# Kernel tuning notes

Hardware: AMD Instinct MI355X
Metric: run time of the kernel (lower is better)

The kernel has to match this reference:

```python
import jax, jax.numpy as jnp
import numpy as np

NZ, N_GEN = 128, 10
H1, H2, IMG = 512, 1024, 784
BATCH = 4096


def setup_inputs() -> dict:
    key = jax.random.key(0)
    ks = jax.random.split(key, 5)
    z = jax.random.normal(ks[0], (BATCH, NZ), dtype=jnp.float32)
    g_idx = jax.random.randint(ks[1], (BATCH,), 0, N_GEN)
    # stacked per-generator MLP weights (fan-in scaled init)
    W1 = jax.random.normal(ks[2], (N_GEN, NZ, H1), dtype=jnp.float32) / np.sqrt(NZ)
    b1 = jnp.zeros((N_GEN, H1), dtype=jnp.float32)
    W2 = jax.random.normal(ks[3], (N_GEN, H1, H2), dtype=jnp.float32) / np.sqrt(H1)
    b2 = jnp.zeros((N_GEN, H2), dtype=jnp.float32)
    W3 = jax.random.normal(ks[4], (N_GEN, H2, IMG), dtype=jnp.float32) / np.sqrt(H2)
    b3 = jnp.zeros((N_GEN, IMG), dtype=jnp.float32)
    return {"z": z, "g_idx": g_idx, "W1": W1, "b1": b1, "W2": W2, "b2": b2, "W3": W3, "b3": b3}


def reference(z, g_idx, W1, b1, W2, b2, W3, b3):
    # Run ALL n_gen sub-generators for every sample (as the torch module does),
    # then gather the chosen branch per sample.
    h = jax.nn.relu(jnp.einsum('bz,gzh->bgh', z, W1) + b1)          # [B, G, H1]
    h = jax.nn.relu(jnp.einsum('bgh,ghk->bgk', h, W2) + b2)         # [B, G, H2]
    images = jnp.tanh(jnp.einsum('bgk,gki->bgi', h, W3) + b3)       # [B, G, IMG]
    # images[arange(B), g_idx]
    out = jnp.take_along_axis(images, g_idx[:, None, None], axis=1)[:, 0]  # [B, IMG]
    return out
```

## Files before the change

### kernel.cpp

```cpp
#include <hip/hip_runtime.h>
#include <math.h>

#define NZ    128
#define H1    512
#define H2    1024
#define IMG   784
#define IMGP  832
#define BATCH 4096
#define NGEN  10
#define MPAD  128

typedef _Float16 f16;
typedef __attribute__((ext_vector_type(8))) _Float16 half8;
typedef __attribute__((ext_vector_type(4))) float floatx4;

__device__ __forceinline__ void cp16(void* l, const void* g) {
    __builtin_amdgcn_global_load_lds((const __attribute__((address_space(1))) void*)g,
                                     (__attribute__((address_space(3))) void*)l, 16, 0, 0);
}

__global__ __launch_bounds__(1024)
void hist_perm(const int* __restrict__ g_idx, int* __restrict__ seg,
               int* __restrict__ perm) {
    __shared__ int lc[NGEN];
    __shared__ int lb[NGEN + 1];
    const int t = threadIdx.x;
    if (t < NGEN) lc[t] = 0;
    __syncthreads();
    int gv[BATCH / 1024];
    #pragma unroll
    for (int i = 0; i < BATCH / 1024; ++i) {
        gv[i] = g_idx[t + i * 1024];
        atomicAdd(&lc[gv[i]], 1);
    }
    __syncthreads();
    if (t == 0) {
        int s = 0;
        for (int g = 0; g < NGEN; ++g) { lb[g] = s; s += lc[g]; }
        lb[NGEN] = s;
    }
    __syncthreads();
    if (t <= NGEN) seg[t] = lb[t];
    if (t < NGEN) lc[t] = lb[t];
    __syncthreads();
    #pragma unroll
    for (int i = 0; i < BATCH / 1024; ++i) {
        int p = atomicAdd(&lc[gv[i]], 1);
        perm[p] = t + i * 1024;
    }
}

__global__ void pack_z(const float* __restrict__ z, const int* __restrict__ perm,
                       f16* __restrict__ zp) {
    const int i = blockIdx.x * 256 + threadIdx.x;
    const int r = i >> 5, c = (i & 31) * 4;
    const int s = perm[r];
    float4 v = *(const float4*)(z + (size_t)s * NZ + c);
    union { ushort4 u; f16 h[4]; } o;
    o.h[0] = (f16)v.x; o.h[1] = (f16)v.y; o.h[2] = (f16)v.z; o.h[3] = (f16)v.w;
    *(ushort4*)(zp + (size_t)r * NZ + c) = o.u;
}

template<int K, int N, int NPAD>
__global__ __launch_bounds__(256)
void transpose_f16(const float* __restrict__ W, f16* __restrict__ Wt) {
    const int g  = blockIdx.z;
    const int k0 = blockIdx.x * 32;
    const int n0 = blockIdx.y * 32;
    __shared__ f16 L[32][36];
    const int t = threadIdx.x;
    {
        const int kk = t >> 3;
        const int nq = (t & 7) * 4;
        float4 v = make_float4(0.f, 0.f, 0.f, 0.f);
        if (n0 + nq < N)
            v = *(const float4*)(W + ((size_t)g * K + (k0 + kk)) * N + n0 + nq);
        L[nq + 0][kk] = (f16)v.x;
        L[nq + 1][kk] = (f16)v.y;
        L[nq + 2][kk] = (f16)v.z;
        L[nq + 3][kk] = (f16)v.w;
    }
    __syncthreads();
    {
        const int nn = t >> 3;
        const int kq = (t & 7) * 4;
        *(ushort4*)(Wt + ((size_t)g * NPAD + (n0 + nn)) * K + k0 + kq) =
            *(const ushort4*)&L[nn][kq];
    }
}

template<int K, int NOUT, int NPADB, int ACT, int SCATTER>
__global__ __launch_bounds__(256)
void gemm64(const f16* __restrict__ Ap, const f16* __restrict__ Wt,
            const float* __restrict__ bias, f16* __restrict__ Ch,
            float* __restrict__ Cout, const int* __restrict__ seg,
            const int* __restrict__ perm) {
    const int g  = blockIdx.z;
    const int s0 = seg[g];
    const int ng = seg[g + 1] - s0;
    const int m0 = blockIdx.x * 64;
    if (m0 >= ng) return;
    const int n0 = blockIdx.y * 64;

    __shared__ f16 As[64 * 64];
    __shared__ f16 Bs[64 * 64];

    const int tid = threadIdx.x, lane = tid & 63, w = tid >> 6;

    const f16* ga[2]; const f16* gb[2]; f16* la[2]; f16* lb[2];
    #pragma unroll
    for (int j = 0; j < 2; ++j) {
        const int r   = w * 16 + j * 8 + (lane >> 3);
        const int swz = ((lane & 7) ^ ((r >> 1) & 7)) * 8;
        ga[j] = Ap + (size_t)(s0 + m0 + r) * K + swz;
        gb[j] = Wt + ((size_t)g * NPADB + n0 + r) * K + swz;
        la[j] = As + (w * 16 + j * 8) * 64;
        lb[j] = Bs + (w * 16 + j * 8) * 64;
    }

    const int wm = (w & 1) * 32, wn = (w >> 1) * 32;
    const int lm = lane & 15, lq = lane >> 4;

    floatx4 acc[2][2] = {};

    #pragma unroll
    for (int kc = 0; kc < K / 64; ++kc) {
        __syncthreads();
        #pragma unroll
        for (int j = 0; j < 2; ++j) {
            cp16(la[j], ga[j]); cp16(lb[j], gb[j]);
            ga[j] += 64; gb[j] += 64;
        }
        __syncthreads();
        #pragma unroll
        for (int ks = 0; ks < 2; ++ks) {
            half8 a[2], b[2];
            #pragma unroll
            for (int mt = 0; mt < 2; ++mt) {
                const int r  = wm + mt * 16 + lm;
                const int pq = (ks * 4 + lq) ^ ((r >> 1) & 7);
                a[mt] = *(const half8*)&As[r * 64 + pq * 8];
            }
            #pragma unroll
            for (int nf = 0; nf < 2; ++nf) {
                const int r  = wn + 2 * lm + nf;
                const int pq = (ks * 4 + lq) ^ ((r >> 1) & 7);
                b[nf] = *(const half8*)&Bs[r * 64 + pq * 8];
            }
            #pragma unroll
            for (int mt = 0; mt < 2; ++mt)
                #pragma unroll
                for (int nf = 0; nf < 2; ++nf)
                    acc[mt][nf] = __builtin_amdgcn_mfma_f32_16x16x32_f16(
                        a[mt], b[nf], acc[mt][nf], 0, 0, 0);
        }
    }

    const int c = n0 + wn + 2 * lm;
    const float b0 = (c     < NOUT) ? bias[(size_t)g * NOUT + c]     : 0.f;
    const float b1 = (c + 1 < NOUT) ? bias[(size_t)g * NOUT + c + 1] : 0.f;
    #pragma unroll
    for (int mt = 0; mt < 2; ++mt)
        #pragma unroll
        for (int rr = 0; rr < 4; ++rr) {
            const int gr = m0 + wm + mt * 16 + lq * 4 + rr;
            if (gr >= ng) continue;
            float x0 = acc[mt][0][rr] + b0;
            float x1 = acc[mt][1][rr] + b1;
            if (ACT == 0) {
                x0 = fmaxf(x0, 0.f); x1 = fmaxf(x1, 0.f);
            } else {
                const float e0 = __expf(2.f * x0);
                const float e1 = __expf(2.f * x1);
                x0 = 1.f - 2.f / (e0 + 1.f);
                x1 = 1.f - 2.f / (e1 + 1.f);
            }
            if (SCATTER) {
                if (c < NOUT) {
                    const size_t orow = (size_t)perm[s0 + gr];
                    *(float2*)&Cout[orow * NOUT + c] = make_float2(x0, x1);
                }
            } else {
                union { uint u; f16 h[2]; } o;
                o.h[0] = (f16)x0; o.h[1] = (f16)x1;
                *(uint*)&Ch[(size_t)(s0 + gr) * NOUT + c] = o.u;
            }
        }
}

extern "C" void kernel_launch(void* const* d_in, const int* in_sizes, int n_in,
                              void* d_out, int out_size, void* d_ws, size_t ws_size,
                              hipStream_t stream) {
    const float* z    = (const float*)d_in[0];
    const int*   gidx = (const int*)  d_in[1];
    const float* W1   = (const float*)d_in[2];
    const float* b1   = (const float*)d_in[3];
    const float* W2   = (const float*)d_in[4];
    const float* b2   = (const float*)d_in[5];
    const float* W3   = (const float*)d_in[6];
    const float* b3   = (const float*)d_in[7];
    float* out = (float*)d_out;

    char* ws = (char*)d_ws;
    size_t off = 0;
    auto alloc = [&](size_t bytes) { size_t o = off; off = (off + bytes + 255) & ~255ULL; return o; };
    int* seg  = (int*)(ws + alloc((size_t)(NGEN + 1) * 4));
    int* perm = (int*)(ws + alloc((size_t)(BATCH + MPAD) * 4));
    f16* zp  = (f16*)(ws + alloc((size_t)(BATCH + MPAD) * NZ * 2));
    f16* h1p = (f16*)(ws + alloc((size_t)(BATCH + MPAD) * H1 * 2));
    f16* h2p = (f16*)(ws + alloc((size_t)(BATCH + MPAD) * H2 * 2));
    f16* W1t = (f16*)(ws + alloc((size_t)NGEN * H1 * NZ * 2));
    f16* W2t = (f16*)(ws + alloc((size_t)NGEN * H2 * H1 * 2));
    f16* W3t = (f16*)(ws + alloc((size_t)NGEN * IMGP * H2 * 2));

    hist_perm<<<dim3(1), dim3(1024), 0, stream>>>(gidx, seg, perm);
    pack_z<<<dim3(BATCH * (NZ / 4) / 256), dim3(256), 0, stream>>>(z, perm, zp);
    transpose_f16<NZ, H1, H1><<<dim3(NZ / 32, H1 / 32, NGEN), dim3(256), 0, stream>>>(W1, W1t);
    transpose_f16<H1, H2, H2><<<dim3(H1 / 32, H2 / 32, NGEN), dim3(256), 0, stream>>>(W2, W2t);
    transpose_f16<H2, IMG, IMGP><<<dim3(H2 / 32, IMGP / 32, NGEN), dim3(256), 0, stream>>>(W3, W3t);

    gemm64<NZ, H1, H1, 0, 0><<<dim3(16, H1 / 64, NGEN), dim3(256), 0, stream>>>(
        zp, W1t, b1, h1p, nullptr, seg, perm);
    gemm64<H1, H2, H2, 0, 0><<<dim3(16, H2 / 64, NGEN), dim3(256), 0, stream>>>(
        h1p, W2t, b2, h2p, nullptr, seg, perm);
    gemm64<H2, IMG, IMGP, 1, 1><<<dim3(16, IMGP / 64, NGEN), dim3(256), 0, stream>>>(
        h2p, W3t, b3, nullptr, out, seg, perm);
}
```

Measured before the change: 181.2 us.

## Double-buffer GEMM LDS tiles and merge weight transposes into one launch

The GEMM main loop now uses two LDS buffers per operand. It prefetches the next K-chunk with global_load_lds while the current one feeds the MFMAs, and uses explicit waitcnt and barriers in place of the two __syncthreads per iteration. The three per-layer weight transpose kernels are fused into a single launch that dispatches tiles by block index. This targets global-load latency inside the GEMMs and the overhead of separate launches. In exchange it doubles LDS use per block and relies on hand-coded waitcnt immediates being correct.

After: 187.3 us. +3.4%, slower.

```diff
diff --git a/kernel.cpp b/kernel.cpp
--- a/kernel.cpp
+++ b/kernel.cpp
@@ -62,11 +62,10 @@
 }
 
 template<int K, int N, int NPAD>
-__global__ __launch_bounds__(256)
-void transpose_f16(const float* __restrict__ W, f16* __restrict__ Wt) {
-    const int g  = blockIdx.z;
-    const int k0 = blockIdx.x * 32;
-    const int n0 = blockIdx.y * 32;
+__device__ __forceinline__
+void trans_tile(const float* __restrict__ W, f16* __restrict__ Wt,
+                int kb, int nb, int g) {
+    const int k0 = kb * 32, n0 = nb * 32;
     __shared__ f16 L[32][36];
     const int t = threadIdx.x;
     {
@@ -89,12 +88,33 @@
     }
 }
 
+#define T1 ((NZ / 32) * (H1 / 32))
+#define T2 ((H1 / 32) * (H2 / 32))
+#define T3 ((H2 / 32) * (IMGP / 32))
+__global__ __launch_bounds__(256)
+void transpose_all(const float* __restrict__ W1, const float* __restrict__ W2,
+                   const float* __restrict__ W3, f16* __restrict__ W1t,
+                   f16* __restrict__ W2t, f16* __restrict__ W3t) {
+    const int g = blockIdx.z;
+    const int x = blockIdx.x;
+    if (x < T1) {
+        trans_tile<NZ, H1, H1>(W1, W1t, x % (NZ / 32), x / (NZ / 32), g);
+    } else if (x < T1 + T2) {
+        const int t = x - T1;
+        trans_tile<H1, H2, H2>(W2, W2t, t % (H1 / 32), t / (H1 / 32), g);
+    } else {
+        const int t = x - T1 - T2;
+        trans_tile<H2, IMG, IMGP>(W3, W3t, t % (H2 / 32), t / (H2 / 32), g);
+    }
+}
+
 template<int K, int NOUT, int NPADB, int ACT, int SCATTER>
 __global__ __launch_bounds__(256)
 void gemm64(const f16* __restrict__ Ap, const f16* __restrict__ Wt,
             const float* __restrict__ bias, f16* __restrict__ Ch,
             float* __restrict__ Cout, const int* __restrict__ seg,
             const int* __restrict__ perm) {
+    constexpr int NI = K / 64;
     const int g  = blockIdx.z;
     const int s0 = seg[g];
     const int ng = seg[g + 1] - s0;
@@ -102,20 +122,19 @@
     if (m0 >= ng) return;
     const int n0 = blockIdx.y * 64;
 
-    __shared__ f16 As[64 * 64];
-    __shared__ f16 Bs[64 * 64];
+    __shared__ f16 As[2][64 * 64];
+    __shared__ f16 Bs[2][64 * 64];
 
     const int tid = threadIdx.x, lane = tid & 63, w = tid >> 6;
 
-    const f16* ga[2]; const f16* gb[2]; f16* la[2]; f16* lb[2];
+    const f16* ga[2]; const f16* gb[2]; int lofs[2];
     #pragma unroll
     for (int j = 0; j < 2; ++j) {
         const int r   = w * 16 + j * 8 + (lane >> 3);
         const int swz = ((lane & 7) ^ ((r >> 1) & 7)) * 8;
         ga[j] = Ap + (size_t)(s0 + m0 + r) * K + swz;
         gb[j] = Wt + ((size_t)g * NPADB + n0 + r) * K + swz;
-        la[j] = As + (w * 16 + j * 8) * 64;
-        lb[j] = Bs + (w * 16 + j * 8) * 64;
+        lofs[j] = (w * 16 + j * 8) * 64;
     }
 
     const int wm = (w & 1) * 32, wn = (w >> 1) * 32;
@@ -124,14 +143,27 @@
     floatx4 acc[2][2] = {};
 
     #pragma unroll
-    for (int kc = 0; kc < K / 64; ++kc) {
-        __syncthreads();
-        #pragma unroll
-        for (int j = 0; j < 2; ++j) {
-            cp16(la[j], ga[j]); cp16(lb[j], gb[j]);
-            ga[j] += 64; gb[j] += 64;
+    for (int j = 0; j < 2; ++j) {
+        cp16(&As[0][lofs[j]], ga[j]); cp16(&Bs[0][lofs[j]], gb[j]);
+    }
+
+    #pragma unroll
+    for (int kc = 0; kc < NI; ++kc) {
+        __builtin_amdgcn_s_barrier();
+        if (kc + 1 < NI) {
+            const int nb = (kc + 1) & 1;
+            #pragma unroll
+            for (int j = 0; j < 2; ++j) {
+                cp16(&As[nb][lofs[j]], ga[j] + (kc + 1) * 64);
+                cp16(&Bs[nb][lofs[j]], gb[j] + (kc + 1) * 64);
+            }
+            __builtin_amdgcn_s_waitcnt(0x0F74);
+        } else {
+            __builtin_amdgcn_s_waitcnt(0x0F70);
         }
-        __syncthreads();
+        __builtin_amdgcn_s_barrier();
+        const f16* AsB = As[kc & 1];
+        const f16* BsB = Bs[kc & 1];
         #pragma unroll
         for (int ks = 0; ks < 2; ++ks) {
             half8 a[2], b[2];
@@ -139,13 +171,13 @@
             for (int mt = 0; mt < 2; ++mt) {
                 const int r  = wm + mt * 16 + lm;
                 const int pq = (ks * 4 + lq) ^ ((r >> 1) & 7);
-                a[mt] = *(const half8*)&As[r * 64 + pq * 8];
+                a[mt] = *(const half8*)&AsB[r * 64 + pq * 8];
             }
             #pragma unroll
             for (int nf = 0; nf < 2; ++nf) {
                 const int r  = wn + 2 * lm + nf;
                 const int pq = (ks * 4 + lq) ^ ((r >> 1) & 7);
-                b[nf] = *(const half8*)&Bs[r * 64 + pq * 8];
+                b[nf] = *(const half8*)&BsB[r * 64 + pq * 8];
             }
             #pragma unroll
             for (int mt = 0; mt < 2; ++mt)
@@ -215,9 +247,8 @@
 
     hist_perm<<<dim3(1), dim3(1024), 0, stream>>>(gidx, seg, perm);
     pack_z<<<dim3(BATCH * (NZ / 4) / 256), dim3(256), 0, stream>>>(z, perm, zp);
-    transpose_f16<NZ, H1, H1><<<dim3(NZ / 32, H1 / 32, NGEN), dim3(256), 0, stream>>>(W1, W1t);
-    transpose_f16<H1, H2, H2><<<dim3(H1 / 32, H2 / 32, NGEN), dim3(256), 0, stream>>>(W2, W2t);
-    transpose_f16<H2, IMG, IMGP><<<dim3(H2 / 32, IMGP / 32, NGEN), dim3(256), 0, stream>>>(W3, W3t);
+    transpose_all<<<dim3(T1 + T2 + T3, 1, NGEN), dim3(256), 0, stream>>>(
+        W1, W2, W3, W1t, W2t, W3t);
 
     gemm64<NZ, H1, H1, 0, 0><<<dim3(16, H1 / 64, NGEN), dim3(256), 0, stream>>>(
         zp, W1t, b1, h1p, nullptr, seg, perm);
```
